# Optimization experiments

Measured on AMD Instinct MI355X. Metric: run time of the kernel, lower is better.

The kernel has to match this reference:

```python
import jax, jax.numpy as jnp
import numpy as np

N, E, D_EDGE, C, H, W, HID = 10000, 160000, 64, 16, 8, 8, 128


def setup_inputs() -> dict:
    key = jax.random.key(0)
    ks = jax.random.split(key, 7)
    x = jax.random.normal(ks[0], (N, C, H, W), jnp.float32)
    edge_attr = jax.random.normal(ks[1], (E, D_EDGE), jnp.float32)
    edge_index = jax.random.randint(ks[2], (2, E), 0, N, dtype=jnp.int64)
    W1 = jax.random.normal(ks[3], (D_EDGE, HID), jnp.float32) * 0.1
    b1 = jnp.zeros((HID,), jnp.float32)
    W2 = jax.random.normal(ks[4], (HID, 1), jnp.float32) * 0.1
    b2 = jnp.zeros((1,), jnp.float32)
    Wn = jax.random.normal(ks[5], (C, 3 * C), jnp.float32) * 0.1
    bn = jnp.zeros((C,), jnp.float32)
    return dict(x=x, edge_attr=edge_attr, W1=W1, b1=b1, W2=W2, b2=b2,
                Wn=Wn, bn=bn, edge_index=edge_index)


def _masked_scatter_softmax(logits, seg, mask, n):
    # softmax over edges grouped by seg, restricted to mask==True edges.
    # Masked edges get -inf logits -> exp 0 -> zero weight (same math as
    # boolean-indexing the edge subset in the torch original).
    neg = jnp.where(mask[:, None], logits, -jnp.inf)          # [E, 1]
    m = jax.ops.segment_max(neg, seg, num_segments=n)         # [N, 1]
    m = jnp.where(jnp.isfinite(m), m, 0.0)                    # empty segments
    e = jnp.exp(neg - m[seg])                                 # [E, 1], 0 where masked
    s = jax.ops.segment_sum(e, seg, num_segments=n)           # [N, 1]
    return e / jnp.maximum(s[seg], 1e-30)


def _flow(x, logits, row, col, mask, n):
    w = _masked_scatter_softmax(logits, row, mask, n)         # [E, 1]
    msg = x[col] * w[:, :, None, None]                        # [E, C, H, W]
    return jax.ops.segment_sum(msg, row, num_segments=n)      # [N, C, H, W]


def reference(x, edge_attr, W1, b1, W2, b2, Wn, bn, edge_index):
    row, col = edge_index[0], edge_index[1]
    # cls_net: MLP edge classifier producing per-edge logit [E, 1]
    h = jax.nn.relu(edge_attr @ W1 + b1)
    dec_edge_feats = h @ W2 + b2
    n = x.shape[0]
    flow_out = _flow(x, dec_edge_feats, row, col, row < col, n)
    flow_in = _flow(x, dec_edge_feats, row, col, row > col, n)
    flow = jnp.concatenate([x, flow_in, flow_out], axis=1)    # [N, 3C, H, W]
    # node_model: 1x1 conv over channels
    out = jnp.einsum('nchw,oc->nohw', flow, Wn) + bn[None, :, None, None]
    return out, dec_edge_feats
```

## Files before the change

kernel.cpp:

```cpp
#include <hip/hip_runtime.h>

#define N_NODES 10000
#define N_EDGES 160000
#define D_EDGE  64
#define C_CH    16
#define HW      64
#define HID     128
#define NODE_ELEMS 1024
#define NSEG    (2 * N_NODES)
#define CAP     64
#define MLPB    (N_EDGES / 64)
#define QUANTB  2500
#define XPITCH  72

typedef __attribute__((ext_vector_type(8))) short short8;
typedef __attribute__((ext_vector_type(4))) float f32x4;

__device__ __forceinline__ unsigned bf16_rne(float f) {
    unsigned u = __float_as_uint(f);
    return (u + 0x7FFFu + ((u >> 16) & 1u)) >> 16;
}
__device__ __forceinline__ short8 pack_bf16x8(float4 lo, float4 hi) {
    union { unsigned u[4]; short8 s; } r;
    r.u[0] = bf16_rne(lo.x) | (bf16_rne(lo.y) << 16);
    r.u[1] = bf16_rne(lo.z) | (bf16_rne(lo.w) << 16);
    r.u[2] = bf16_rne(hi.x) | (bf16_rne(hi.y) << 16);
    r.u[3] = bf16_rne(hi.z) | (bf16_rne(hi.w) << 16);
    return r.s;
}

__global__ __launch_bounds__(256) void k_prep(
    const float* __restrict__ W1, const float* __restrict__ Wn,
    unsigned short* __restrict__ W1bfT, unsigned short* __restrict__ WnTb,
    unsigned* __restrict__ zbase)
{
    int tid = threadIdx.x;
    if (blockIdx.x < 4) {
        int q  = blockIdx.x * 256 + tid;
        int n  = q >> 3;
        int ko = (q & 7) * 8;
        #pragma unroll
        for (int i = 0; i < 8; ++i) {
            int k = ko + i;
            W1bfT[n * 64 + k] = (unsigned short)bf16_rne(W1[k * HID + n]);
        }
    } else if (blockIdx.x == 4) {
        int q = tid * 4;
        int o = q >> 6, k0 = q & 63;
        #pragma unroll
        for (int i = 0; i < 4; ++i) {
            int k = k0 + i;
            WnTb[o * 64 + k] =
                (k < 48) ? (unsigned short)bf16_rne(Wn[o * 48 + k]) : 0;
        }
    } else {
        int idx = (blockIdx.x - 5) * 256 + tid;
        for (int i = idx; i < NSEG; i += 64 * 256) zbase[i] = 0u;
    }
}

__device__ __forceinline__ unsigned pb4(float4 f, float inv) {
    int a = (int)rintf(f.x * inv) + 128;
    int b = (int)rintf(f.y * inv) + 128;
    int c = (int)rintf(f.z * inv) + 128;
    int d = (int)rintf(f.w * inv) + 128;
    a = min(255, max(0, a)); b = min(255, max(0, b));
    c = min(255, max(0, c)); d = min(255, max(0, d));
    return (unsigned)a | ((unsigned)b << 8) | ((unsigned)c << 16) | ((unsigned)d << 24);
}
__global__ __launch_bounds__(256) void k_mlpcast(
    const float* __restrict__ ea, const unsigned short* __restrict__ W1bfT,
    const float* __restrict__ b1, const float* __restrict__ W2,
    const float* __restrict__ b2,
    const int* __restrict__ row, const int* __restrict__ col,
    const float* __restrict__ x, unsigned char* __restrict__ xq,
    float* __restrict__ scale,
    float* __restrict__ dec,
    int* __restrict__ cursor, int2* __restrict__ bucket)
{
    const int tid = threadIdx.x;

    if (blockIdx.x >= MLPB) {
        const int wv = tid >> 6, ln = tid & 63;
        const int n  = (blockIdx.x - MLPB) * 4 + wv;
        const float4* xs = (const float4*)(x + (size_t)n * NODE_ELEMS) + ln * 4;
        float4 v0 = xs[0], v1 = xs[1], v2 = xs[2], v3 = xs[3];
        float m = fmaxf(fmaxf(fmaxf(fabsf(v0.x), fabsf(v0.y)),
                              fmaxf(fabsf(v0.z), fabsf(v0.w))),
                 fmaxf(fmaxf(fmaxf(fabsf(v1.x), fabsf(v1.y)),
                              fmaxf(fabsf(v1.z), fabsf(v1.w))),
                 fmaxf(fmaxf(fmaxf(fabsf(v2.x), fabsf(v2.y)),
                              fmaxf(fabsf(v2.z), fabsf(v2.w))),
                       fmaxf(fmaxf(fabsf(v3.x), fabsf(v3.y)),
                              fmaxf(fabsf(v3.z), fabsf(v3.w))))));
        #pragma unroll
        for (int off = 1; off < 64; off <<= 1)
            m = fmaxf(m, __shfl_xor(m, off));
        m = fmaxf(m, 1e-20f);
        float inv = 127.0f / m;
        uint4 o;
        o.x = pb4(v0, inv); o.y = pb4(v1, inv);
        o.z = pb4(v2, inv); o.w = pb4(v3, inv);
        ((uint4*)(xq + (size_t)n * NODE_ELEMS))[ln] = o;
        if (ln == 0) scale[n] = m * (1.0f / 127.0f);
        return;
    }

    __shared__ float s_w2[HID], s_b1[HID];
    __shared__ float s_logit[64];

    const int eb = blockIdx.x * 64;

    int e_c = 0, pos = -1, seg = 0;
    if (tid < 64) {
        int e = eb + tid;
        int r = row[e]; e_c = col[e];
        if (r != e_c) {
            seg = 2 * r + ((r < e_c) ? 0 : 1);
            pos = atomicAdd(&cursor[seg], 1);
        }
    }

    if (tid < HID) { s_w2[tid] = W2[tid]; s_b1[tid] = b1[tid]; }

    const int lane = tid & 63, w = tid >> 6;
    const int i15 = lane & 15, g = lane >> 4;
    const int m = w * 16 + i15;

    short8 bfrag[2][8];
    #pragma unroll
    for (int kt = 0; kt < 2; ++kt)
        #pragma unroll
        for (int t = 0; t < 8; ++t)
            bfrag[kt][t] = *(const short8*)&W1bfT[(t * 16 + i15) * 64 + kt * 32 + g * 8];

    short8 afrag[2];
    #pragma unroll
    for (int kt = 0; kt < 2; ++kt) {
        const float4* src = (const float4*)&ea[(size_t)(eb + m) * D_EDGE + kt * 32 + g * 8];
        afrag[kt] = pack_bf16x8(src[0], src[1]);
    }

    f32x4 acc[8];
    #pragma unroll
    for (int t = 0; t < 8; ++t) acc[t] = (f32x4){0.f, 0.f, 0.f, 0.f};
    #pragma unroll
    for (int kt = 0; kt < 2; ++kt)
        #pragma unroll
        for (int t = 0; t < 8; ++t)
            acc[t] = __builtin_amdgcn_mfma_f32_16x16x32_bf16(afrag[kt], bfrag[kt][t],
                                                             acc[t], 0, 0, 0);
    __syncthreads();

    float loc[4] = {0.f, 0.f, 0.f, 0.f};
    #pragma unroll
    for (int t = 0; t < 8; ++t) {
        float w2v = s_w2[t * 16 + i15];
        float bv  = s_b1[t * 16 + i15];
        #pragma unroll
        for (int r = 0; r < 4; ++r)
            loc[r] = fmaf(fmaxf(acc[t][r] + bv, 0.f), w2v, loc[r]);
    }
    #pragma unroll
    for (int r = 0; r < 4; ++r) {
        #pragma unroll
        for (int off = 1; off < 16; off <<= 1)
            loc[r] += __shfl_xor(loc[r], off);
    }
    if (i15 == 0) {
        #pragma unroll
        for (int r = 0; r < 4; ++r)
            s_logit[w * 16 + g * 4 + r] = loc[r];
    }
    __syncthreads();

    if (tid < 64) {
        float logit = s_logit[tid] + b2[0];
        dec[eb + tid] = logit;
        if (pos >= 0 && pos < CAP) {
            float ex = expf(logit);
            bucket[((size_t)seg << 6) + pos] = make_int2(e_c, __float_as_int(ex));
        }
    }
}

__device__ __forceinline__ void acc8(float* A, uint2 v, float ws) {
    A[0] = fmaf(ws, (float)( v.x        & 255u), A[0]);
    A[1] = fmaf(ws, (float)((v.x >>  8) & 255u), A[1]);
    A[2] = fmaf(ws, (float)((v.x >> 16) & 255u), A[2]);
    A[3] = fmaf(ws, (float)( v.x >> 24        ), A[3]);
    A[4] = fmaf(ws, (float)( v.y        & 255u), A[4]);
    A[5] = fmaf(ws, (float)((v.y >>  8) & 255u), A[5]);
    A[6] = fmaf(ws, (float)((v.y >> 16) & 255u), A[6]);
    A[7] = fmaf(ws, (float)( v.y >> 24        ), A[7]);
}

__global__ __launch_bounds__(128) void k_gather(
    const float* __restrict__ x, const unsigned char* __restrict__ xq,
    const float* __restrict__ scale,
    const int* __restrict__ cursor, const int2* __restrict__ bucket,
    const unsigned short* __restrict__ WnTb, const float* __restrict__ bn,
    float* __restrict__ out)
{
    const int n = blockIdx.x;
    const int t = threadIdx.x;

    __shared__ __align__(16) unsigned short sxf[64 * XPITCH];
    __shared__ int2  s_ecw[2 * CAP];
    __shared__ float s_ex[2 * CAP];

    {
        int zr = t >> 1, zk = 48 + (t & 1) * 8;
        *(uint4*)&sxf[zr * XPITCH + zk] = make_uint4(0, 0, 0, 0);
    }

    const int c0  = min(cursor[2 * n],     CAP);
    const int c1  = min(cursor[2 * n + 1], CAP);
    const int tot = c0 + c1;
    if (t < tot) {
        int2 e = (t < c0) ? bucket[((size_t)(2 * n) << 6) + t]
                          : bucket[((size_t)(2 * n + 1) << 6) + t - c0];
        float ex = __int_as_float(e.y);
        s_ex[t] = ex;
        e.y = __float_as_int(ex * scale[e.x]);
        s_ecw[t] = e;
    }
    __syncthreads();

    float sum0 = 0.f, sum1 = 0.f;
    for (int i = 0; i < c0; ++i)   sum0 += s_ex[i];
    for (int i = c0; i < tot; ++i) sum1 += s_ex[i];

    float a[8] = {0,0,0,0,0,0,0,0};
    float b[8] = {0,0,0,0,0,0,0,0};
    float wsA = 0.f, wsB = 0.f;
    const uint2* xqt = (const uint2*)xq + t;

#define FMAJ(J) { float ws = __int_as_float(s_ecw[i + (J)].y);                \
                  if (i + (J) < c0) { acc8(a, v[J], ws); wsA += ws; }         \
                  else              { acc8(b, v[J], ws); wsB += ws; } }

    int i = 0;
    for (; i + 16 <= tot; i += 16) {
        uint2 v[16];
        #pragma unroll
        for (int j = 0; j < 16; ++j) v[j] = xqt[(size_t)s_ecw[i + j].x * 128];
        #pragma unroll
        for (int j = 0; j < 16; ++j) FMAJ(j)
    }
    for (; i + 8 <= tot; i += 8) {
        uint2 v[8];
        #pragma unroll
        for (int j = 0; j < 8; ++j) v[j] = xqt[(size_t)s_ecw[i + j].x * 128];
        #pragma unroll
        for (int j = 0; j < 8; ++j) FMAJ(j)
    }
    for (; i + 4 <= tot; i += 4) {
        uint2 v[4];
        #pragma unroll
        for (int j = 0; j < 4; ++j) v[j] = xqt[(size_t)s_ecw[i + j].x * 128];
        #pragma unroll
        for (int j = 0; j < 4; ++j) FMAJ(j)
    }
    for (; i < tot; ++i) {
        uint2 v[1];
        v[0] = xqt[(size_t)s_ecw[i].x * 128];
        FMAJ(0)
    }
#undef FMAJ

    const int c_of_t = t >> 3, hw0 = (t & 7) * 8;
    const float4* xsrc = (const float4*)(x + (size_t)n * NODE_ELEMS) + t * 2;
    float4 xv0 = xsrc[0], xv1 = xsrc[1];

    const float r0 = 1.0f / fmaxf(sum0, 1e-30f);
    const float r1 = 1.0f / fmaxf(sum1, 1e-30f);
    const float o0 = 128.0f * wsA, o1 = 128.0f * wsB;
    float xv[8] = {xv0.x, xv0.y, xv0.z, xv0.w, xv1.x, xv1.y, xv1.z, xv1.w};
    #pragma unroll
    for (int j = 0; j < 8; ++j) {
        unsigned short* rowp = &sxf[(hw0 + j) * XPITCH];
        rowp[     c_of_t] = (unsigned short)bf16_rne(xv[j]);
        rowp[16 + c_of_t] = (unsigned short)bf16_rne((b[j] - o1) * r1);
        rowp[32 + c_of_t] = (unsigned short)bf16_rne((a[j] - o0) * r0);
    }
    __syncthreads();

    const int lane = t & 63, wv = t >> 6;
    const int i15 = lane & 15, g = lane >> 4;
    const float bno = bn[i15];
    float* outb = out + (size_t)n * NODE_ELEMS;

    #pragma unroll
    for (int mt = 0; mt < 2; ++mt) {
        const int mrow = (wv * 2 + mt) * 16;
        f32x4 accm = (f32x4){bno, bno, bno, bno};
        #pragma unroll
        for (int kt = 0; kt < 2; ++kt) {
            short8 af = *(const short8*)&sxf[(mrow + i15) * XPITCH + kt * 32 + g * 8];
            short8 bf = *(const short8*)&WnTb[i15 * 64 + kt * 32 + g * 8];
            accm = __builtin_amdgcn_mfma_f32_16x16x32_bf16(af, bf, accm, 0, 0, 0);
        }
        const int hwb = mrow + g * 4;
        #pragma unroll
        for (int r = 0; r < 4; ++r)
            outb[i15 * 64 + hwb + r] = accm[r];
    }
}

extern "C" void kernel_launch(void* const* d_in, const int* in_sizes, int n_in,
                              void* d_out, int out_size, void* d_ws, size_t ws_size,
                              hipStream_t stream)
{
    const float* x         = (const float*)d_in[0];
    const float* edge_attr = (const float*)d_in[1];
    const float* W1        = (const float*)d_in[2];
    const float* b1        = (const float*)d_in[3];
    const float* W2        = (const float*)d_in[4];
    const float* b2        = (const float*)d_in[5];
    const float* Wn        = (const float*)d_in[6];
    const float* bn        = (const float*)d_in[7];
    const int*   eidx      = (const int*)d_in[8];
    const int*   row       = eidx;
    const int*   col       = eidx + N_EDGES;

    float* out = (float*)d_out;
    float* dec = out + (size_t)N_NODES * NODE_ELEMS;

    unsigned char* xq     = (unsigned char*)d_ws;
    float*         scale  = (float*)(xq + (size_t)N_NODES * NODE_ELEMS);
    int2*          bucket = (int2*)(scale + N_NODES);
    int*           cursor = (int*)(bucket + (size_t)NSEG * CAP);
    unsigned short* W1bfT = (unsigned short*)(cursor + NSEG);
    unsigned short* WnTb  = W1bfT + D_EDGE * HID;

    k_prep<<<69, 256, 0, stream>>>(W1, Wn, W1bfT, WnTb, (unsigned*)cursor);
    k_mlpcast<<<MLPB + QUANTB, 256, 0, stream>>>(edge_attr, W1bfT, b1, W2, b2,
                                                 row, col, x, xq, scale,
                                                 dec, cursor, bucket);
    k_gather<<<N_NODES, 128, 0, stream>>>(x, xq, scale, cursor,
                                          bucket, WnTb, bn, out);
}
```

Before: 80.89 us.

## Process more edges and nodes per block with register-resident weights and prefetch

The fused MLP/quantize kernel now gives each wave 64 edges, processed as four 16-edge MFMA tiles, so each block covers 256 edges instead of 64. This amortizes the W1 fragment loads and the W2/b1 loads, which now live in registers instead of shared memory, and removes both __syncthreads. Logits are combined with lane shuffles instead of through shared memory. The quantize path gives each wave four nodes with double-buffered prefetch of the next node's data. The cost is fewer blocks in flight (625+625 instead of 2500+2500), which lowers parallelism and latency hiding, and higher register pressure.

```diff
diff --git a/kernel.cpp b/kernel.cpp
--- a/kernel.cpp
+++ b/kernel.cpp
@@ -9,8 +9,8 @@
 #define NODE_ELEMS 1024
 #define NSEG    (2 * N_NODES)
 #define CAP     64
-#define MLPB    (N_EDGES / 64)
-#define QUANTB  2500
+#define MLPB    625
+#define QUANTB  625
 #define XPITCH  72
 
 typedef __attribute__((ext_vector_type(8))) short short8;
@@ -78,108 +78,136 @@
     float* __restrict__ dec,
     int* __restrict__ cursor, int2* __restrict__ bucket)
 {
-    const int tid = threadIdx.x;
+    const int tid  = threadIdx.x;
+    const int lane = tid & 63, wv = tid >> 6;
 
     if (blockIdx.x >= MLPB) {
-        const int wv = tid >> 6, ln = tid & 63;
-        const int n  = (blockIdx.x - MLPB) * 4 + wv;
-        const float4* xs = (const float4*)(x + (size_t)n * NODE_ELEMS) + ln * 4;
-        float4 v0 = xs[0], v1 = xs[1], v2 = xs[2], v3 = xs[3];
-        float m = fmaxf(fmaxf(fmaxf(fabsf(v0.x), fabsf(v0.y)),
-                              fmaxf(fabsf(v0.z), fabsf(v0.w))),
-                 fmaxf(fmaxf(fmaxf(fabsf(v1.x), fabsf(v1.y)),
-                              fmaxf(fabsf(v1.z), fabsf(v1.w))),
-                 fmaxf(fmaxf(fmaxf(fabsf(v2.x), fabsf(v2.y)),
-                              fmaxf(fabsf(v2.z), fabsf(v2.w))),
-                       fmaxf(fmaxf(fabsf(v3.x), fabsf(v3.y)),
-                              fmaxf(fabsf(v3.z), fabsf(v3.w))))));
-        #pragma unroll
-        for (int off = 1; off < 64; off <<= 1)
-            m = fmaxf(m, __shfl_xor(m, off));
-        m = fmaxf(m, 1e-20f);
-        float inv = 127.0f / m;
-        uint4 o;
-        o.x = pb4(v0, inv); o.y = pb4(v1, inv);
-        o.z = pb4(v2, inv); o.w = pb4(v3, inv);
-        ((uint4*)(xq + (size_t)n * NODE_ELEMS))[ln] = o;
-        if (ln == 0) scale[n] = m * (1.0f / 127.0f);
+        const int nb = (blockIdx.x - MLPB) * 16 + wv * 4;
+        const int ln = lane;
+        float4 v[2][4];
+        {
+            const float4* xs = (const float4*)(x + (size_t)nb * NODE_ELEMS) + ln * 4;
+            v[0][0] = xs[0]; v[0][1] = xs[1]; v[0][2] = xs[2]; v[0][3] = xs[3];
+        }
+        #pragma unroll
+        for (int j = 0; j < 4; ++j) {
+            if (j < 3) {
+                const float4* xs =
+                    (const float4*)(x + (size_t)(nb + j + 1) * NODE_ELEMS) + ln * 4;
+                v[(j + 1) & 1][0] = xs[0]; v[(j + 1) & 1][1] = xs[1];
+                v[(j + 1) & 1][2] = xs[2]; v[(j + 1) & 1][3] = xs[3];
+            }
+            float4 v0 = v[j & 1][0], v1 = v[j & 1][1];
+            float4 v2 = v[j & 1][2], v3 = v[j & 1][3];
+            float m = fmaxf(fmaxf(fmaxf(fabsf(v0.x), fabsf(v0.y)),
+                                  fmaxf(fabsf(v0.z), fabsf(v0.w))),
+                     fmaxf(fmaxf(fmaxf(fabsf(v1.x), fabsf(v1.y)),
+                                  fmaxf(fabsf(v1.z), fabsf(v1.w))),
+                     fmaxf(fmaxf(fmaxf(fabsf(v2.x), fabsf(v2.y)),
+                                  fmaxf(fabsf(v2.z), fabsf(v2.w))),
+                           fmaxf(fmaxf(fabsf(v3.x), fabsf(v3.y)),
+                                  fmaxf(fabsf(v3.z), fabsf(v3.w))))));
+            #pragma unroll
+            for (int off = 1; off < 64; off <<= 1)
+                m = fmaxf(m, __shfl_xor(m, off));
+            m = fmaxf(m, 1e-20f);
+            float inv = 127.0f / m;
+            uint4 o;
+            o.x = pb4(v0, inv); o.y = pb4(v1, inv);
+            o.z = pb4(v2, inv); o.w = pb4(v3, inv);
+            ((uint4*)(xq + (size_t)(nb + j) * NODE_ELEMS))[ln] = o;
+            if (ln == 0) scale[nb + j] = m * (1.0f / 127.0f);
+        }
         return;
     }
 
-    __shared__ float s_w2[HID], s_b1[HID];
-    __shared__ float s_logit[64];
-
-    const int eb = blockIdx.x * 64;
-
-    int e_c = 0, pos = -1, seg = 0;
-    if (tid < 64) {
-        int e = eb + tid;
-        int r = row[e]; e_c = col[e];
-        if (r != e_c) {
-            seg = 2 * r + ((r < e_c) ? 0 : 1);
-            pos = atomicAdd(&cursor[seg], 1);
-        }
-    }
-
-    if (tid < HID) { s_w2[tid] = W2[tid]; s_b1[tid] = b1[tid]; }
-
-    const int lane = tid & 63, w = tid >> 6;
     const int i15 = lane & 15, g = lane >> 4;
-    const int m = w * 16 + i15;
+    const int ebase = blockIdx.x * 256 + wv * 64;
+
+    int e_c[4], seg[4], pos[4];
+    if (lane < 16) {
+        #pragma unroll
+        for (int t = 0; t < 4; ++t) {
+            int e = ebase + t * 16 + lane;
+            int r = row[e], c = col[e];
+            e_c[t] = c; pos[t] = -1; seg[t] = 0;
+            if (r != c) {
+                seg[t] = 2 * r + ((r < c) ? 0 : 1);
+                pos[t] = atomicAdd(&cursor[seg[t]], 1);
+            }
+        }
+    }
+
+    float w2v[8], bv[8];
+    #pragma unroll
+    for (int t8 = 0; t8 < 8; ++t8) {
+        w2v[t8] = W2[t8 * 16 + i15];
+        bv[t8]  = b1[t8 * 16 + i15];
+    }
+    const float b2v = b2[0];
 
     short8 bfrag[2][8];
     #pragma unroll
     for (int kt = 0; kt < 2; ++kt)
         #pragma unroll
-        for (int t = 0; t < 8; ++t)
-            bfrag[kt][t] = *(const short8*)&W1bfT[(t * 16 + i15) * 64 + kt * 32 + g * 8];
-
-    short8 afrag[2];
+        for (int t8 = 0; t8 < 8; ++t8)
+            bfrag[kt][t8] =
+                *(const short8*)&W1bfT[(t8 * 16 + i15) * 64 + kt * 32 + g * 8];
+
+    short8 aF[2][2];
     #pragma unroll
     for (int kt = 0; kt < 2; ++kt) {
-        const float4* src = (const float4*)&ea[(size_t)(eb + m) * D_EDGE + kt * 32 + g * 8];
-        afrag[kt] = pack_bf16x8(src[0], src[1]);
-    }
-
-    f32x4 acc[8];
-    #pragma unroll
-    for (int t = 0; t < 8; ++t) acc[t] = (f32x4){0.f, 0.f, 0.f, 0.f};
-    #pragma unroll
-    for (int kt = 0; kt < 2; ++kt)
-        #pragma unroll
-        for (int t = 0; t < 8; ++t)
-            acc[t] = __builtin_amdgcn_mfma_f32_16x16x32_bf16(afrag[kt], bfrag[kt][t],
-                                                             acc[t], 0, 0, 0);
-    __syncthreads();
-
-    float loc[4] = {0.f, 0.f, 0.f, 0.f};
-    #pragma unroll
-    for (int t = 0; t < 8; ++t) {
-        float w2v = s_w2[t * 16 + i15];
-        float bv  = s_b1[t * 16 + i15];
-        #pragma unroll
-        for (int r = 0; r < 4; ++r)
-            loc[r] = fmaf(fmaxf(acc[t][r] + bv, 0.f), w2v, loc[r]);
-    }
-    #pragma unroll
-    for (int r = 0; r < 4; ++r) {
-        #pragma unroll
-        for (int off = 1; off < 16; off <<= 1)
-            loc[r] += __shfl_xor(loc[r], off);
-    }
-    if (i15 == 0) {
-        #pragma unroll
-        for (int r = 0; r < 4; ++r)
-            s_logit[w * 16 + g * 4 + r] = loc[r];
-    }
-    __syncthreads();
-
-    if (tid < 64) {
-        float logit = s_logit[tid] + b2[0];
-        dec[eb + tid] = logit;
-        if (pos >= 0 && pos < CAP) {
-            float ex = expf(logit);
-            bucket[((size_t)seg << 6) + pos] = make_int2(e_c, __float_as_int(ex));
+        const float4* src =
+            (const float4*)&ea[(size_t)(ebase + i15) * D_EDGE + kt * 32 + g * 8];
+        aF[0][kt] = pack_bf16x8(src[0], src[1]);
+    }
+
+    #pragma unroll
+    for (int t = 0; t < 4; ++t) {
+        if (t < 3) {
+            #pragma unroll
+            for (int kt = 0; kt < 2; ++kt) {
+                const float4* src = (const float4*)
+                    &ea[(size_t)(ebase + (t + 1) * 16 + i15) * D_EDGE + kt * 32 + g * 8];
+                aF[(t + 1) & 1][kt] = pack_bf16x8(src[0], src[1]);
+            }
+        }
+        f32x4 acc[8];
+        #pragma unroll
+        for (int t8 = 0; t8 < 8; ++t8) acc[t8] = (f32x4){0.f, 0.f, 0.f, 0.f};
+        #pragma unroll
+        for (int kt = 0; kt < 2; ++kt)
+            #pragma unroll
+            for (int t8 = 0; t8 < 8; ++t8)
+                acc[t8] = __builtin_amdgcn_mfma_f32_16x16x32_bf16(
+                    aF[t & 1][kt], bfrag[kt][t8], acc[t8], 0, 0, 0);
+
+        float loc[4] = {0.f, 0.f, 0.f, 0.f};
+        #pragma unroll
+        for (int t8 = 0; t8 < 8; ++t8) {
+            #pragma unroll
+            for (int r = 0; r < 4; ++r)
+                loc[r] = fmaf(fmaxf(acc[t8][r] + bv[t8], 0.f), w2v[t8], loc[r]);
+        }
+        #pragma unroll
+        for (int r = 0; r < 4; ++r) {
+            #pragma unroll
+            for (int off = 1; off < 16; off <<= 1)
+                loc[r] += __shfl_xor(loc[r], off);
+        }
+        int srcl = ((lane & 15) >> 2) << 4;
+        float t0 = __shfl(loc[0], srcl), t1 = __shfl(loc[1], srcl);
+        float t2 = __shfl(loc[2], srcl), t3 = __shfl(loc[3], srcl);
+        if (lane < 16) {
+            int rr = lane & 3;
+            float logit = ((rr == 0) ? t0 : (rr == 1) ? t1 : (rr == 2) ? t2 : t3)
+                          + b2v;
+            dec[ebase + t * 16 + lane] = logit;
+            if (pos[t] >= 0 && pos[t] < CAP) {
+                float ex = expf(logit);
+                bucket[((size_t)seg[t] << 6) + pos[t]] =
+                    make_int2(e_c[t], __float_as_int(ex));
+            }
         }
     }
 }
```

New measurement: 75.38 us. 6.8% less time.
